# Performance work log

Measured on AMD Instinct MI355X. Metric: run time of the kernel, lower is better.

## Reference

```python
import jax, jax.numpy as jnp
import numpy as np

B, T, C = 4, 2048, 1024
H = 16
D = C // H  # 64


def setup_inputs() -> dict:
    key = jax.random.key(0)
    ks = jax.random.split(key, 4)
    s = 0.02
    return {
        "x": jax.random.normal(ks[0], (B, T, C), dtype=jnp.float32),
        "w_qkv": jax.random.normal(ks[1], (C, 3 * C), dtype=jnp.float32) * s,
        "b_qkv": jnp.zeros((3 * C,), dtype=jnp.float32),
        "w_proj": jax.random.normal(ks[2], (C, C), dtype=jnp.float32) * s,
        "b_proj": jnp.zeros((C,), dtype=jnp.float32),
    }


def reference(x, w_qkv, b_qkv, w_proj, b_proj):
    Bx, Tx, Cx = x.shape
    qkv = x @ w_qkv + b_qkv                     # [B,T,3C]
    q, k, v = jnp.split(qkv, 3, axis=-1)
    # [B,T,C] -> [B,H,T,D]
    def heads(t):
        return t.reshape(Bx, Tx, H, D).transpose(0, 2, 1, 3)
    q, k, v = heads(q), heads(k), heads(v)
    scale = 1.0 / jnp.sqrt(jnp.float32(D))
    att = jnp.einsum("bhqd,bhkd->bhqk", q, k) * scale
    causal = jnp.tril(jnp.ones((Tx, Tx), dtype=bool))
    att = jnp.where(causal[None, None], att, -jnp.inf)
    att = jax.nn.softmax(att, axis=-1)
    y = jnp.einsum("bhqk,bhkd->bhqd", att, v)   # [B,H,T,D]
    y = y.transpose(0, 2, 1, 3).reshape(Bx, Tx, Cx)
    return y @ w_proj + b_proj
```

## Files before the change

### kernel.cpp

```cpp
#include <hip/hip_runtime.h>
#include <hip/hip_bf16.h>
#include <cstdint>
#include <cstddef>

#define BB 4
#define TT 2048
#define CC 1024
#define HH 16
#define DD 64
#define MM (BB*TT)

typedef short bf16x8 __attribute__((ext_vector_type(8)));
typedef float f32x4 __attribute__((ext_vector_type(4)));

typedef const __attribute__((address_space(1))) void GV;
typedef __attribute__((address_space(3))) void LV;
#define GLL16(g, l) __builtin_amdgcn_global_load_lds((GV*)(g), (LV*)(l), 16, 0, 0)

__device__ __forceinline__ short f2b(float f) {
  __hip_bfloat16 h = __float2bfloat16(f);
  return *reinterpret_cast<short*>(&h);
}

__global__ void cvt_kernel(const float* __restrict__ in, short* __restrict__ out, int n4) {
  int i = blockIdx.x * blockDim.x + threadIdx.x;
  if (i < n4) {
    float4 v = ((const float4*)in)[i];
    short4 o;
    o.x = f2b(v.x); o.y = f2b(v.y); o.z = f2b(v.z); o.w = f2b(v.w);
    ((short4*)out)[i] = o;
  }
}

__global__ void transpose_cvt(const float* __restrict__ in, short* __restrict__ out,
                              int K, int N) {
  __shared__ short t[32][33];
  int n0 = blockIdx.x * 32, k0 = blockIdx.y * 32;
  int tx = threadIdx.x, ty = threadIdx.y;
  #pragma unroll
  for (int r = ty; r < 32; r += 8)
    t[r][tx] = f2b(in[(size_t)(k0 + r) * N + n0 + tx]);
  __syncthreads();
  #pragma unroll
  for (int r = ty; r < 32; r += 8)
    out[(size_t)(n0 + r) * K + k0 + tx] = t[tx][r];
}

template<int EPI>
__global__ __launch_bounds__(256)
void gemm_bf16(const short* __restrict__ A, const short* __restrict__ Bt,
               const float* __restrict__ bias, int M, int N, int K,
               short* __restrict__ Qb, short* __restrict__ Kb, short* __restrict__ Vt,
               float* __restrict__ Cout)
{
  constexpr int BK = 32;
  __shared__ short As[128 * BK];
  __shared__ short Bs[128 * BK];
  const int tid = threadIdx.x;
  const int lane = tid & 63, wave = tid >> 6;
  const int g = lane >> 4, qq = lane & 15;
  const int gx = gridDim.x;
  int flat = blockIdx.y * gx + blockIdx.x;
  int cpx = (gx * gridDim.y) >> 3;
  int swz = (flat & 7) * cpx + (flat >> 3);
  const int m0 = (swz / gx) * 128, n0 = (swz % gx) * 128;
  const int wr = wave >> 1, wc = wave & 1;

  f32x4 acc[4][4] = {};
  for (int k0 = 0; k0 < K; k0 += BK) {
    __syncthreads();
    #pragma unroll
    for (int i = 0; i < 2; ++i) {
      int id = i * 256 + tid; int row = id >> 2, off = id & 3;
      GLL16(A + (size_t)(m0 + row) * K + k0 + off * 8, As + id * 8);
    }
    #pragma unroll
    for (int i = 0; i < 2; ++i) {
      int id = i * 256 + tid; int row = id >> 2, off = id & 3;
      GLL16(Bt + (size_t)(n0 + row) * K + k0 + off * 8, Bs + id * 8);
    }
    __syncthreads();
    bf16x8 af[4], bfr[4];
    #pragma unroll
    for (int mi = 0; mi < 4; ++mi)
      af[mi] = *(const bf16x8*)(As + (wr * 64 + mi * 16 + qq) * BK + g * 8);
    #pragma unroll
    for (int ni = 0; ni < 4; ++ni)
      bfr[ni] = *(const bf16x8*)(Bs + (wc * 64 + ni * 16 + qq) * BK + g * 8);
    #pragma unroll
    for (int mi = 0; mi < 4; ++mi)
      #pragma unroll
      for (int ni = 0; ni < 4; ++ni)
        acc[mi][ni] = __builtin_amdgcn_mfma_f32_16x16x32_bf16(af[mi], bfr[ni], acc[mi][ni], 0, 0, 0);
  }

  const int brow = m0 + wr * 64, bcol = n0 + wc * 64;
  #pragma unroll
  for (int ni = 0; ni < 4; ++ni) {
    int n = bcol + ni * 16 + qq;
    float bs = bias[n];
    if (EPI == 0) {
      int sec = n >> 10, cc = n & 1023, h = cc >> 6, d = cc & 63;
      float qscale = (sec == 0) ? 0.125f : 1.0f;
      #pragma unroll
      for (int mi = 0; mi < 4; ++mi) {
        int t0 = brow + mi * 16 + g * 4;
        int b = t0 >> 11, tt = t0 & 2047;
        if (sec == 2) {
          size_t base = ((size_t)(b * HH + h) * DD + d) * TT + tt;
          short4 o;
          o.x = f2b(acc[mi][ni][0] + bs); o.y = f2b(acc[mi][ni][1] + bs);
          o.z = f2b(acc[mi][ni][2] + bs); o.w = f2b(acc[mi][ni][3] + bs);
          *(short4*)(Vt + base) = o;
        } else {
          short* dst = (sec == 0) ? Qb : Kb;
          size_t base = ((size_t)(b * HH + h) * TT + tt) * DD + d;
          #pragma unroll
          for (int r = 0; r < 4; ++r)
            dst[base + (size_t)r * DD] = f2b((acc[mi][ni][r] + bs) * qscale);
        }
      }
    } else {
      #pragma unroll
      for (int mi = 0; mi < 4; ++mi) {
        int t0 = brow + mi * 16 + g * 4;
        #pragma unroll
        for (int r = 0; r < 4; ++r)
          Cout[(size_t)(t0 + r) * N + n] = acc[mi][ni][r] + bs;
      }
    }
  }
}

__global__ __launch_bounds__(256, 2)
void attn_kernel(const short* __restrict__ Qb, const short* __restrict__ Kb,
                 const short* __restrict__ Vt, short* __restrict__ Yout)
{
  __shared__ short Kbuf[2][64 * 64];
  __shared__ short Vbuf[2][64 * 64];
  __shared__ short Plds[4][16 * 64];
  const int bid = blockIdx.x;
  const int bh = bid & 63;
  const int qt = 15 - (bid >> 6);
  const int tid = threadIdx.x, w = tid >> 6, lane = tid & 63;
  const int g = lane >> 4, qq = lane & 15;
  const size_t headQK = (size_t)bh * TT * DD;
  const size_t headV  = (size_t)bh * DD * TT;
  const int q0 = qt * 128;
  const int nt = 2 * qt + 2;
  const int sw = (qq & 7) << 4;
  const float FIXM = 6.0f;

#define STAGE(bufi, kv0_) do {                                                   \
    int id0 = tid; int row0 = id0 >> 3;                                          \
    int so0 = ((((id0 & 7) * 16) ^ ((row0 & 7) << 4)) >> 1);                     \
    GLL16(Kb + headQK + (size_t)((kv0_) + row0) * DD + so0, &Kbuf[bufi][0] + id0 * 8); \
    GLL16(Vt + headV + (size_t)row0 * TT + (kv0_) + so0, &Vbuf[bufi][0] + id0 * 8);    \
    int id1 = 256 + tid; int row1 = id1 >> 3;                                    \
    int so1 = ((((id1 & 7) * 16) ^ ((row1 & 7) << 4)) >> 1);                     \
    GLL16(Kb + headQK + (size_t)((kv0_) + row1) * DD + so1, &Kbuf[bufi][0] + id1 * 8); \
    GLL16(Vt + headV + (size_t)row1 * TT + (kv0_) + so1, &Vbuf[bufi][0] + id1 * 8);    \
  } while (0)

  bf16x8 qf[2][2];
  #pragma unroll
  for (int qt2 = 0; qt2 < 2; ++qt2) {
    int qrow = q0 + qt2 * 64 + w * 16 + qq;
    qf[qt2][0] = *(const bf16x8*)(Qb + headQK + (size_t)qrow * DD + g * 8);
    qf[qt2][1] = *(const bf16x8*)(Qb + headQK + (size_t)qrow * DD + 32 + g * 8);
  }

  f32x4 yacc[2][4] = {};
  float l_run[2] = { 0.f, 0.f };
  char* pb = (char*)&Plds[w][0];

  STAGE(0, 0);

  for (int kt = 0; kt < nt; ++kt) {
    const int p = kt & 1;
    const int kv0 = kt * 64;
    if (kt + 1 < nt) {
      STAGE(p ^ 1, kv0 + 64);
      asm volatile("s_waitcnt vmcnt(4)" ::: "memory");
    } else {
      asm volatile("s_waitcnt vmcnt(0)" ::: "memory");
    }
    __builtin_amdgcn_s_barrier();
    __builtin_amdgcn_sched_barrier(0);

    const char* kbase = (const char*)&Kbuf[p][0];
    const char* vbase = (const char*)&Vbuf[p][0];
    const bool skip0 = (kv0 > q0 + w * 16 + 15);

    f32x4 sa[2][4] = {};
    __builtin_amdgcn_s_setprio(1);
    #pragma unroll
    for (int kb = 0; kb < 4; ++kb) {
      int lrow = kb * 16 + qq;
      bf16x8 kf0 = *(const bf16x8*)(kbase + lrow * 128 + ((g * 16) ^ sw));
      bf16x8 kf1 = *(const bf16x8*)(kbase + lrow * 128 + ((64 + g * 16) ^ sw));
      if (!skip0) {
        sa[0][kb] = __builtin_amdgcn_mfma_f32_16x16x32_bf16(kf0, qf[0][0], sa[0][kb], 0, 0, 0);
        sa[0][kb] = __builtin_amdgcn_mfma_f32_16x16x32_bf16(kf1, qf[0][1], sa[0][kb], 0, 0, 0);
      }
      sa[1][kb] = __builtin_amdgcn_mfma_f32_16x16x32_bf16(kf0, qf[1][0], sa[1][kb], 0, 0, 0);
      sa[1][kb] = __builtin_amdgcn_mfma_f32_16x16x32_bf16(kf1, qf[1][1], sa[1][kb], 0, 0, 0);
    }
    __builtin_amdgcn_s_setprio(0);

    bf16x8 vf[4][2];
    #pragma unroll
    for (int db = 0; db < 4; ++db) {
      int lrow = db * 16 + qq;
      vf[db][0] = *(const bf16x8*)(vbase + lrow * 128 + ((g * 16) ^ sw));
      vf[db][1] = *(const bf16x8*)(vbase + lrow * 128 + ((64 + g * 16) ^ sw));
    }

    #pragma unroll
    for (int qt2 = 0; qt2 < 2; ++qt2) {
      if (qt2 == 0 && skip0) continue;
      const int qsb = q0 + qt2 * 64 + w * 16;
      const bool need_mask = (kv0 + 63 > qsb);
      const int qcol = qsb + qq;

      float p16[16]; float ls = 0.f;
      #pragma unroll
      for (int kb = 0; kb < 4; ++kb)
        #pragma unroll
        for (int r = 0; r < 4; ++r) {
          float v = sa[qt2][kb][r];
          if (need_mask) {
            int key = kv0 + kb * 16 + g * 4 + r;
            if (key > qcol) v = -INFINITY;
          }
          float e = __expf(v - FIXM);
          p16[kb * 4 + r] = e;
          ls += e;
        }
      l_run[qt2] += ls;

      #pragma unroll
      for (int kb = 0; kb < 4; ++kb) {
        short4 o;
        o.x = f2b(p16[kb * 4 + 0]); o.y = f2b(p16[kb * 4 + 1]);
        o.z = f2b(p16[kb * 4 + 2]); o.w = f2b(p16[kb * 4 + 3]);
        int wb = qq * 128 + ((kb * 32 + g * 8) ^ sw);
        *(short4*)(pb + wb) = o;
      }

      __builtin_amdgcn_s_setprio(1);
      #pragma unroll
      for (int kk = 0; kk < 2; ++kk) {
        int rb = qq * 128 + ((kk * 64 + g * 16) ^ sw);
        bf16x8 pf = *(const bf16x8*)(pb + rb);
        #pragma unroll
        for (int db = 0; db < 4; ++db)
          yacc[qt2][db] = __builtin_amdgcn_mfma_f32_16x16x32_bf16(pf, vf[db][kk], yacc[qt2][db], 0, 0, 0);
      }
      __builtin_amdgcn_s_setprio(0);
    }

    __builtin_amdgcn_sched_barrier(0);
    __builtin_amdgcn_s_barrier();
  }
#undef STAGE

  const int b = bh >> 4, h = bh & 15;
  #pragma unroll
  for (int qt2 = 0; qt2 < 2; ++qt2) {
    float lt = l_run[qt2];
    lt += __shfl_xor(lt, 16);
    lt += __shfl_xor(lt, 32);
    float li[4];
    #pragma unroll
    for (int r = 0; r < 4; ++r) li[r] = 1.f / __shfl(lt, g * 4 + r);
    #pragma unroll
    for (int db = 0; db < 4; ++db)
      #pragma unroll
      for (int r = 0; r < 4; ++r) {
        int t = q0 + qt2 * 64 + w * 16 + g * 4 + r;
        Yout[((size_t)(b * TT + t)) * CC + h * DD + db * 16 + qq] = f2b(yacc[qt2][db][r] * li[r]);
      }
  }
}

extern "C" void kernel_launch(void* const* d_in, const int* in_sizes, int n_in,
                              void* d_out, int out_size, void* d_ws, size_t ws_size,
                              hipStream_t stream)
{
  const float* x      = (const float*)d_in[0];
  const float* w_qkv  = (const float*)d_in[1];
  const float* b_qkv  = (const float*)d_in[2];
  const float* w_proj = (const float*)d_in[3];
  const float* b_proj = (const float*)d_in[4];
  float* out = (float*)d_out;

  short* ws     = (short*)d_ws;
  short* xb     = ws;
  short* wqkvT  = ws + 8388608;
  short* wprojT = ws + 11534336;
  short* Qb     = ws + 12582912;
  short* Kb     = ws + 20971520;
  short* Vt     = ws + 29360128;

  hipLaunchKernelGGL(cvt_kernel, dim3(8192), dim3(256), 0, stream, x, xb, 2097152);
  hipLaunchKernelGGL(transpose_cvt, dim3(96, 32), dim3(32, 8), 0, stream, w_qkv, wqkvT, 1024, 3072);
  hipLaunchKernelGGL(transpose_cvt, dim3(32, 32), dim3(32, 8), 0, stream, w_proj, wprojT, 1024, 1024);
  hipLaunchKernelGGL((gemm_bf16<0>), dim3(24, 64), dim3(256), 0, stream,
                     xb, wqkvT, b_qkv, MM, 3 * CC, CC, Qb, Kb, Vt, (float*)nullptr);
  hipLaunchKernelGGL(attn_kernel, dim3(1024), dim3(256), 0, stream, Qb, Kb, Vt, xb);
  hipLaunchKernelGGL((gemm_bf16<1>), dim3(8, 64), dim3(256), 0, stream,
                     xb, wprojT, b_proj, MM, CC, CC, (short*)nullptr, (short*)nullptr, (short*)nullptr, out);
}
```

Before: 188.9 us.

## Rewrite GEMM with BK=64 multi-buffered async loads and exp2 softmax

The GEMM kernel now uses 512-thread blocks with 128x256 tiles and a K step of 64. A and B tiles are prefetched into double- and triple-buffered XOR-swizzled LDS with explicit vmcnt waits, and MFMA is issued at raised priority. Separately, log2(e) is folded into the Q scale so attention can use exp2f with a rescaled fixed max instead of __expf. This targets load latency stalls, LDS bank conflicts and per-element exp cost, at the price of a much larger LDS footprint that may limit occupancy.

```diff
diff --git a/kernel.cpp b/kernel.cpp
--- a/kernel.cpp
+++ b/kernel.cpp
@@ -47,52 +47,92 @@
 }
 
 template<int EPI>
-__global__ __launch_bounds__(256)
-void gemm_bf16(const short* __restrict__ A, const short* __restrict__ Bt,
+__global__ __launch_bounds__(512, 2)
+void gemm_bk64(const short* __restrict__ A, const short* __restrict__ Bt,
                const float* __restrict__ bias, int M, int N, int K,
                short* __restrict__ Qb, short* __restrict__ Kb, short* __restrict__ Vt,
                float* __restrict__ Cout)
 {
-  constexpr int BK = 32;
-  __shared__ short As[128 * BK];
-  __shared__ short Bs[128 * BK];
+  __shared__ short As[2][128 * 64];
+  __shared__ short Bs[3][256 * 64];
   const int tid = threadIdx.x;
-  const int lane = tid & 63, wave = tid >> 6;
+  const int lane = tid & 63, w = tid >> 6;
   const int g = lane >> 4, qq = lane & 15;
+  const int wr = w >> 2, wc = w & 3;
   const int gx = gridDim.x;
   int flat = blockIdx.y * gx + blockIdx.x;
   int cpx = (gx * gridDim.y) >> 3;
   int swz = (flat & 7) * cpx + (flat >> 3);
-  const int m0 = (swz / gx) * 128, n0 = (swz % gx) * 128;
-  const int wr = wave >> 1, wc = wave & 1;
-
+  const int m0 = (swz / gx) * 128, n0 = (swz % gx) * 256;
+
+  const int crow = tid >> 3, cslot = tid & 7;
+  const int sca = (cslot ^ (crow & 7)) * 8;
+  char* ABb = (char*)&As[0][0];
+  char* BBb = (char*)&Bs[0][0];
+
+#define STG_A(b, kt_) do {                                                          \
+    GLL16(A + (size_t)(m0 + crow) * K + (kt_) * 64 + sca,                           \
+          ABb + (b) * 16384 + tid * 16);                                            \
+    GLL16(A + (size_t)(m0 + crow + 64) * K + (kt_) * 64 + sca,                      \
+          ABb + (b) * 16384 + (512 + tid) * 16);                                    \
+  } while (0)
+#define STG_B(b, kt_) do {                                                          \
+    GLL16(Bt + (size_t)(n0 + crow) * K + (kt_) * 64 + sca,                          \
+          BBb + (b) * 32768 + tid * 16);                                            \
+    GLL16(Bt + (size_t)(n0 + crow + 64) * K + (kt_) * 64 + sca,                     \
+          BBb + (b) * 32768 + (512 + tid) * 16);                                    \
+    GLL16(Bt + (size_t)(n0 + 128 + crow) * K + (kt_) * 64 + sca,                    \
+          BBb + (b) * 32768 + 16384 + tid * 16);                                    \
+    GLL16(Bt + (size_t)(n0 + 128 + crow + 64) * K + (kt_) * 64 + sca,               \
+          BBb + (b) * 32768 + 16384 + (512 + tid) * 16);                            \
+  } while (0)
+
+  const int NT = K >> 6;
+  const int rsw = (qq & 7) << 4;
   f32x4 acc[4][4] = {};
-  for (int k0 = 0; k0 < K; k0 += BK) {
-    __syncthreads();
-    #pragma unroll
-    for (int i = 0; i < 2; ++i) {
-      int id = i * 256 + tid; int row = id >> 2, off = id & 3;
-      GLL16(A + (size_t)(m0 + row) * K + k0 + off * 8, As + id * 8);
-    }
-    #pragma unroll
-    for (int i = 0; i < 2; ++i) {
-      int id = i * 256 + tid; int row = id >> 2, off = id & 3;
-      GLL16(Bt + (size_t)(n0 + row) * K + k0 + off * 8, Bs + id * 8);
-    }
-    __syncthreads();
-    bf16x8 af[4], bfr[4];
+
+  STG_A(0, 0); STG_B(0, 0); STG_B(1, 1);
+  int rbB = 0, sbB = 2;
+  for (int kt = 0; kt < NT; ++kt) {
+    if (kt + 1 < NT) asm volatile("s_waitcnt vmcnt(4)" ::: "memory");
+    else             asm volatile("s_waitcnt vmcnt(0)" ::: "memory");
+    __builtin_amdgcn_s_barrier();
+    __builtin_amdgcn_sched_barrier(0);
+    if (kt + 1 < NT) STG_A((kt + 1) & 1, kt + 1);
+    if (kt + 2 < NT) STG_B(sbB, kt + 2);
+
+    const char* ab = ABb + (kt & 1) * 16384;
+    const char* bb = BBb + rbB * 32768;
+    bf16x8 af[4][2], bfr[4][2];
     #pragma unroll
     for (int mi = 0; mi < 4; ++mi)
-      af[mi] = *(const bf16x8*)(As + (wr * 64 + mi * 16 + qq) * BK + g * 8);
+      #pragma unroll
+      for (int kk = 0; kk < 2; ++kk)
+        af[mi][kk] = *(const bf16x8*)(ab + (wr * 64 + mi * 16 + qq) * 128 + ((kk * 64 + g * 16) ^ rsw));
     #pragma unroll
     for (int ni = 0; ni < 4; ++ni)
-      bfr[ni] = *(const bf16x8*)(Bs + (wc * 64 + ni * 16 + qq) * BK + g * 8);
+      #pragma unroll
+      for (int kk = 0; kk < 2; ++kk)
+        bfr[ni][kk] = *(const bf16x8*)(bb + (wc * 64 + ni * 16 + qq) * 128 + ((kk * 64 + g * 16) ^ rsw));
+
+    __builtin_amdgcn_s_setprio(1);
     #pragma unroll
     for (int mi = 0; mi < 4; ++mi)
       #pragma unroll
-      for (int ni = 0; ni < 4; ++ni)
-        acc[mi][ni] = __builtin_amdgcn_mfma_f32_16x16x32_bf16(af[mi], bfr[ni], acc[mi][ni], 0, 0, 0);
-  }
+      for (int ni = 0; ni < 4; ++ni) {
+        acc[mi][ni] = __builtin_amdgcn_mfma_f32_16x16x32_bf16(af[mi][0], bfr[ni][0], acc[mi][ni], 0, 0, 0);
+        acc[mi][ni] = __builtin_amdgcn_mfma_f32_16x16x32_bf16(af[mi][1], bfr[ni][1], acc[mi][ni], 0, 0, 0);
+      }
+    __builtin_amdgcn_s_setprio(0);
+
+    asm volatile("s_waitcnt lgkmcnt(0)" ::: "memory");
+    __builtin_amdgcn_sched_barrier(0);
+
+    rbB = (rbB == 2) ? 0 : rbB + 1;
+    sbB = (sbB == 2) ? 0 : sbB + 1;
+  }
+#undef STG_A
+#undef STG_B
 
   const int brow = m0 + wr * 64, bcol = n0 + wc * 64;
   #pragma unroll
@@ -101,7 +141,7 @@
     float bs = bias[n];
     if (EPI == 0) {
       int sec = n >> 10, cc = n & 1023, h = cc >> 6, d = cc & 63;
-      float qscale = (sec == 0) ? 0.125f : 1.0f;
+      float qscale = (sec == 0) ? 0.18033688f : 1.0f;
       #pragma unroll
       for (int mi = 0; mi < 4; ++mi) {
         int t0 = brow + mi * 16 + g * 4;
@@ -149,7 +189,7 @@
   const int q0 = qt * 128;
   const int nt = 2 * qt + 2;
   const int sw = (qq & 7) << 4;
-  const float FIXM = 6.0f;
+  const float FIXM2 = 8.65617025f;
 
 #define STAGE(bufi, kv0_) do {                                                   \
     int id0 = tid; int row0 = id0 >> 3;                                          \
@@ -233,7 +273,7 @@
             int key = kv0 + kb * 16 + g * 4 + r;
             if (key > qcol) v = -INFINITY;
           }
-          float e = __expf(v - FIXM);
+          float e = exp2f(v - FIXM2);
           p16[kb * 4 + r] = e;
           ls += e;
         }
@@ -306,9 +346,9 @@
   hipLaunchKernelGGL(cvt_kernel, dim3(8192), dim3(256), 0, stream, x, xb, 2097152);
   hipLaunchKernelGGL(transpose_cvt, dim3(96, 32), dim3(32, 8), 0, stream, w_qkv, wqkvT, 1024, 3072);
   hipLaunchKernelGGL(transpose_cvt, dim3(32, 32), dim3(32, 8), 0, stream, w_proj, wprojT, 1024, 1024);
-  hipLaunchKernelGGL((gemm_bf16<0>), dim3(24, 64), dim3(256), 0, stream,
+  hipLaunchKernelGGL((gemm_bk64<0>), dim3(12, 64), dim3(512), 0, stream,
                      xb, wqkvT, b_qkv, MM, 3 * CC, CC, Qb, Kb, Vt, (float*)nullptr);
   hipLaunchKernelGGL(attn_kernel, dim3(1024), dim3(256), 0, stream, Qb, Kb, Vt, xb);
-  hipLaunchKernelGGL((gemm_bf16<1>), dim3(8, 64), dim3(256), 0, stream,
+  hipLaunchKernelGGL((gemm_bk64<1>), dim3(4, 64), dim3(512), 0, stream,
                      xb, wprojT, b_proj, MM, CC, CC, (short*)nullptr, (short*)nullptr, (short*)nullptr, out);
 }
```

Measured after the change: 196.2 us. 3.9% more time.
